# Kernel optimization log

Measured on AMD Instinct MI355X. Metric: run time of the kernel, lower is better.

The kernel has to match this reference:

```python
import jax, jax.numpy as jnp
import numpy as np

N_HEAD = 4

def setup_inputs() -> dict:
    key = jax.random.key(0)
    ks = jax.random.split(key, 5)
    B, T, C = 2, 4096, 64
    return {
        "x": jax.random.normal(ks[0], (B, T, C), dtype=jnp.float32),
        "w_attn": jax.random.normal(ks[1], (3 * C, C), dtype=jnp.float32) * 0.02,
        "b_attn": jax.random.normal(ks[2], (3 * C,), dtype=jnp.float32) * 0.02,
        "w_proj": jax.random.normal(ks[3], (C, C), dtype=jnp.float32) * 0.02,
        "b_proj": jax.random.normal(ks[4], (C,), dtype=jnp.float32) * 0.02,
    }

def reference(x, w_attn, b_attn, w_proj, b_proj):
    B, T, C = x.shape
    H = N_HEAD
    Dh = C // H
    # fused QKV projection (torch Linear: x @ W.T + b)
    qkv = x @ w_attn.T + b_attn                      # [B,T,3C]
    q, k, v = jnp.split(qkv, 3, axis=-1)             # each [B,T,C]
    q = q.reshape(B, T, H, Dh).transpose(0, 2, 1, 3)  # [B,H,T,Dh]
    k = k.reshape(B, T, H, Dh).transpose(0, 2, 1, 3)
    v = v.reshape(B, T, H, Dh).transpose(0, 2, 1, 3)
    scale = 1.0 / np.sqrt(Dh).astype(np.float32)
    scores = jnp.einsum("bhqd,bhkd->bhqk", q, k) * scale  # [B,H,T,T]
    attn = jax.nn.softmax(scores, axis=-1)
    y = jnp.einsum("bhqk,bhkd->bhqd", attn, v)       # [B,H,T,Dh]
    y = y.transpose(0, 2, 1, 3).reshape(B, T, C)     # [B,T,C]
    return y @ w_proj.T + b_proj
```

## Files before the change

### kernel.cpp

```cpp
#include <hip/hip_runtime.h>
#include <math.h>

#define BB 2
#define TT 4096
#define CC 64
#define HH 4
#define DH 16
#define NROW (BB*TT)
#define SCALE 0.36067376022224085f

typedef __fp16 h4 __attribute__((ext_vector_type(4)));
typedef __fp16 h2 __attribute__((ext_vector_type(2)));
typedef float  f4 __attribute__((ext_vector_type(4)));

__global__ __launch_bounds__(256) void qkv_kernel(const float* __restrict__ x,
        const float* __restrict__ w, const float* __restrict__ bias,
        __fp16* __restrict__ Q, __fp16* __restrict__ K, __fp16* __restrict__ VT) {
    __shared__ __fp16 smv[64][16];
    const int t = threadIdx.x;
    const int wave = t >> 6, lane = t & 63;
    const int lq = lane & 15, g = lane >> 4;
    const int r0 = blockIdx.x*16;
    const int b = r0 >> 12, tt0 = r0 & (TT-1);

    h4 xb[4];
    const float* xrow = x + (size_t)(r0 + lq)*CC;
    #pragma unroll
    for (int s = 0; s < 4; s++) {
        float4 xv = *(const float4*)(xrow + s*16 + g*4);
        h2 lo = __builtin_amdgcn_cvt_pkrtz(xv.x, xv.y);
        h2 hi = __builtin_amdgcn_cvt_pkrtz(xv.z, xv.w);
        xb[s] = (h4){lo.x, lo.y, hi.x, hi.y};
    }

    #pragma unroll
    for (int j = 0; j < 3; j++) {
        const int nt = wave*3 + j;
        const int o0 = nt*16;
        const float sc = (nt < 4) ? SCALE : 1.0f;
        float4 bv = *(const float4*)(bias + o0 + g*4);
        f4 acc = {bv.x*sc, bv.y*sc, bv.z*sc, bv.w*sc};
        #pragma unroll
        for (int s = 0; s < 4; s++) {
            float4 wv = *(const float4*)(w + (size_t)(o0 + lq)*CC + s*16 + g*4);
            h2 lo = __builtin_amdgcn_cvt_pkrtz(wv.x*sc, wv.y*sc);
            h2 hi = __builtin_amdgcn_cvt_pkrtz(wv.z*sc, wv.w*sc);
            h4 af = (h4){lo.x, lo.y, hi.x, hi.y};
            acc = __builtin_amdgcn_mfma_f32_16x16x16f16(af, xb[s], acc, 0, 0, 0);
        }
        h2 plo = __builtin_amdgcn_cvt_pkrtz(acc.x, acc.y);
        h2 phi = __builtin_amdgcn_cvt_pkrtz(acc.z, acc.w);
        h4 pk = (h4){plo.x, plo.y, phi.x, phi.y};
        if (nt < 8) {
            const int part = nt >> 2, h = nt & 3;
            __fp16* dst = (part == 0) ? Q : K;
            *(h4*)(dst + ((size_t)(b*HH + h)*TT + tt0 + lq)*DH + g*4) = pk;
        } else {
            const int h = nt - 8;
            smv[h*16 + g*4 + 0][lq] = pk.x;
            smv[h*16 + g*4 + 1][lq] = pk.y;
            smv[h*16 + g*4 + 2][lq] = pk.z;
            smv[h*16 + g*4 + 3][lq] = pk.w;
        }
    }
    __syncthreads();
    if (t < 64) {
        const int h = t >> 4, d = t & 15;
        uint4 v0 = *(const uint4*)&smv[t][0];
        uint4 v1 = *(const uint4*)&smv[t][8];
        __fp16* dst = VT + (size_t)(b*HH + h)*TT*DH
                        + (size_t)((tt0 >> 6)*16 + d)*64 + (tt0 & 63);
        *(uint4*)dst = v0;
        *(uint4*)(dst + 8) = v1;
    }
}

__global__ __launch_bounds__(256) void attn_kernel(const __fp16* __restrict__ Q,
        const __fp16* __restrict__ K, const __fp16* __restrict__ VT,
        __fp16* __restrict__ yh) {
    __shared__ f4    Osm[4][4][64];
    __shared__ float Lsm[4][4][64];
    const int t = threadIdx.x;
    const int wave = t >> 6, lane = t & 63;
    const int lq = lane & 15, g = lane >> 4;
    const int head = blockIdx.x >> 6;
    const int qt   = blockIdx.x & 63;
    const int q0 = qt*64;
    const __fp16* Qh = Q  + (size_t)head*TT*DH;
    const __fp16* Kh = K  + (size_t)head*TT*DH;
    const __fp16* Vh = VT + (size_t)head*TT*DH;

    h4 qf[4];
    #pragma unroll
    for (int h = 0; h < 4; h++)
        qf[h] = *(const h4*)(Qh + (size_t)(q0 + h*16 + lq)*DH + g*4);

    f4 O[4];
    float lp[4];
    #pragma unroll
    for (int h = 0; h < 4; h++) { O[h] = (f4){0.f,0.f,0.f,0.f}; lp[h] = 0.f; }

    const __fp16* kbase = Kh + (size_t)(wave*1024 + lq)*DH + g*4;
    const __fp16* vbase = Vh + (size_t)(wave*16)*1024 + lq*64 + g*4;

    const int start = (blockIdx.x*5 + wave*3) & 15;

    h4 ka[4], va[4], kb[4], vb[4];
    {
        const int c0 = start;
        #pragma unroll
        for (int s = 0; s < 4; s++) {
            ka[s] = *(const h4*)(kbase + (size_t)c0*64*DH + (size_t)s*16*DH);
            va[s] = *(const h4*)(vbase + (size_t)c0*1024 + s*16);
        }
    }

#define ATTN_CHUNK(KF, VF)                                                        \
    {                                                                             \
        const f4 z = {0.f, 0.f, 0.f, 0.f};                                        \
        _Pragma("unroll")                                                         \
        for (int h = 0; h < 4; h++) {                                             \
            f4 S0 = __builtin_amdgcn_mfma_f32_16x16x16f16(KF[0], qf[h], z, 0,0,0);\
            f4 S1 = __builtin_amdgcn_mfma_f32_16x16x16f16(KF[1], qf[h], z, 0,0,0);\
            f4 S2 = __builtin_amdgcn_mfma_f32_16x16x16f16(KF[2], qf[h], z, 0,0,0);\
            f4 S3 = __builtin_amdgcn_mfma_f32_16x16x16f16(KF[3], qf[h], z, 0,0,0);\
            float p0, p1, p2, p3; h2 lo, hi; h4 P; float lacc = 0.f;              \
            p0 = __builtin_amdgcn_exp2f(S0.x); p1 = __builtin_amdgcn_exp2f(S0.y); \
            p2 = __builtin_amdgcn_exp2f(S0.z); p3 = __builtin_amdgcn_exp2f(S0.w); \
            lacc += p0 + p1 + p2 + p3;                                            \
            lo = __builtin_amdgcn_cvt_pkrtz(p0, p1);                              \
            hi = __builtin_amdgcn_cvt_pkrtz(p2, p3);                              \
            P = (h4){lo.x, lo.y, hi.x, hi.y};                                     \
            O[h] = __builtin_amdgcn_mfma_f32_16x16x16f16(VF[0], P, O[h], 0,0,0);  \
            p0 = __builtin_amdgcn_exp2f(S1.x); p1 = __builtin_amdgcn_exp2f(S1.y); \
            p2 = __builtin_amdgcn_exp2f(S1.z); p3 = __builtin_amdgcn_exp2f(S1.w); \
            lacc += p0 + p1 + p2 + p3;                                            \
            lo = __builtin_amdgcn_cvt_pkrtz(p0, p1);                              \
            hi = __builtin_amdgcn_cvt_pkrtz(p2, p3);                              \
            P = (h4){lo.x, lo.y, hi.x, hi.y};                                     \
            O[h] = __builtin_amdgcn_mfma_f32_16x16x16f16(VF[1], P, O[h], 0,0,0);  \
            p0 = __builtin_amdgcn_exp2f(S2.x); p1 = __builtin_amdgcn_exp2f(S2.y); \
            p2 = __builtin_amdgcn_exp2f(S2.z); p3 = __builtin_amdgcn_exp2f(S2.w); \
            lacc += p0 + p1 + p2 + p3;                                            \
            lo = __builtin_amdgcn_cvt_pkrtz(p0, p1);                              \
            hi = __builtin_amdgcn_cvt_pkrtz(p2, p3);                              \
            P = (h4){lo.x, lo.y, hi.x, hi.y};                                     \
            O[h] = __builtin_amdgcn_mfma_f32_16x16x16f16(VF[2], P, O[h], 0,0,0);  \
            p0 = __builtin_amdgcn_exp2f(S3.x); p1 = __builtin_amdgcn_exp2f(S3.y); \
            p2 = __builtin_amdgcn_exp2f(S3.z); p3 = __builtin_amdgcn_exp2f(S3.w); \
            lacc += p0 + p1 + p2 + p3;                                            \
            lo = __builtin_amdgcn_cvt_pkrtz(p0, p1);                              \
            hi = __builtin_amdgcn_cvt_pkrtz(p2, p3);                              \
            P = (h4){lo.x, lo.y, hi.x, hi.y};                                     \
            O[h] = __builtin_amdgcn_mfma_f32_16x16x16f16(VF[3], P, O[h], 0,0,0);  \
            lp[h] += lacc;                                                        \
        }                                                                         \
    }

    for (int it = 0; it < 16; it += 2) {
        {
            const int c1 = (start + it + 1) & 15;
            #pragma unroll
            for (int s = 0; s < 4; s++) {
                kb[s] = *(const h4*)(kbase + (size_t)c1*64*DH + (size_t)s*16*DH);
                vb[s] = *(const h4*)(vbase + (size_t)c1*1024 + s*16);
            }
        }
        ATTN_CHUNK(ka, va)
        {
            const int c2 = (start + it + 2) & 15;
            #pragma unroll
            for (int s = 0; s < 4; s++) {
                ka[s] = *(const h4*)(kbase + (size_t)c2*64*DH + (size_t)s*16*DH);
                va[s] = *(const h4*)(vbase + (size_t)c2*1024 + s*16);
            }
        }
        ATTN_CHUNK(kb, vb)
    }
#undef ATTN_CHUNK

    #pragma unroll
    for (int h = 0; h < 4; h++) {
        Osm[wave][h][lane] = O[h];
        Lsm[wave][h][lane] = lp[h];
    }
    __syncthreads();

    f4 Os = Osm[0][wave][lane];
    Os += Osm[1][wave][lane];
    Os += Osm[2][wave][lane];
    Os += Osm[3][wave][lane];
    float L = 0.f;
    #pragma unroll
    for (int ks = 0; ks < 4; ks++)
        #pragma unroll
        for (int gg = 0; gg < 4; gg++)
            L += Lsm[ks][wave][gg*16 + lq];
    const float rinv = 1.f / L;
    h2 lo = __builtin_amdgcn_cvt_pkrtz(Os.x*rinv, Os.y*rinv);
    h2 hi = __builtin_amdgcn_cvt_pkrtz(Os.z*rinv, Os.w*rinv);
    h4 pk = (h4){lo.x, lo.y, hi.x, hi.y};
    const int b = head >> 2, hh = head & 3;
    *(h4*)(yh + ((size_t)b*TT + q0 + wave*16 + lq)*CC + hh*DH + g*4) = pk;
}

__global__ __launch_bounds__(256) void proj_kernel(const __fp16* __restrict__ yh,
        const float* __restrict__ w, const float* __restrict__ bias,
        float* __restrict__ out) {
    const int t = threadIdx.x;
    const int wave = t >> 6, lane = t & 63;
    const int lq = lane & 15, g = lane >> 4;
    const int r0 = blockIdx.x*16;
    const int o0 = wave*16;

    h4 yb[4];
    const __fp16* yrow = yh + (size_t)(r0 + lq)*CC;
    #pragma unroll
    for (int s = 0; s < 4; s++) yb[s] = *(const h4*)(yrow + s*16 + g*4);

    float4 bv = *(const float4*)(bias + o0 + g*4);
    f4 acc = {bv.x, bv.y, bv.z, bv.w};
    #pragma unroll
    for (int s = 0; s < 4; s++) {
        float4 wv = *(const float4*)(w + (size_t)(o0 + lq)*CC + s*16 + g*4);
        h2 lo = __builtin_amdgcn_cvt_pkrtz(wv.x, wv.y);
        h2 hi = __builtin_amdgcn_cvt_pkrtz(wv.z, wv.w);
        h4 af = (h4){lo.x, lo.y, hi.x, hi.y};
        acc = __builtin_amdgcn_mfma_f32_16x16x16f16(af, yb[s], acc, 0, 0, 0);
    }
    *(float4*)(out + (size_t)(r0 + lq)*CC + o0 + g*4) = (float4){acc.x, acc.y, acc.z, acc.w};
}

extern "C" void kernel_launch(void* const* d_in, const int* in_sizes, int n_in,
                              void* d_out, int out_size, void* d_ws, size_t ws_size,
                              hipStream_t stream) {
    const float* x      = (const float*)d_in[0];
    const float* w_attn = (const float*)d_in[1];
    const float* b_attn = (const float*)d_in[2];
    const float* w_proj = (const float*)d_in[3];
    const float* b_proj = (const float*)d_in[4];
    float* out = (float*)d_out;

    const size_t headsz = (size_t)BB*HH*TT*DH;
    __fp16* Q   = (__fp16*)d_ws;
    __fp16* K   = Q + headsz;
    __fp16* VT  = K + headsz;
    __fp16* yh  = VT + headsz;

    qkv_kernel<<<NROW/16, 256, 0, stream>>>(x, w_attn, b_attn, Q, K, VT);
    attn_kernel<<<BB*HH*(TT/64), 256, 0, stream>>>(Q, K, VT, yh);
    proj_kernel<<<NROW/16, 256, 0, stream>>>(yh, w_proj, b_proj, out);
}
```

Baseline: 95.16 us.

## Switch attention to 32x32x16 MFMA with ones-padded V for fused row sums

Rewrites the attention inner loop to use 32x32x16 f16 MFMA tiles instead of 16x16x16. S accumulators are rearranged into B-operand layout with v_permlane32_swap. The V^T buffer is padded to 32 rows per tile, with constant-one rows written in the qkv kernel, so the softmax denominator comes out of the PV MFMA instead of scalar adds. This aims to raise matrix throughput per instruction and drop the separate row-sum accumulation, at the cost of twice the V storage and bandwidth and wasted MFMA lanes on padding rows.

```diff
diff --git a/kernel.cpp b/kernel.cpp
--- a/kernel.cpp
+++ b/kernel.cpp
@@ -11,7 +11,12 @@
 
 typedef __fp16 h4 __attribute__((ext_vector_type(4)));
 typedef __fp16 h2 __attribute__((ext_vector_type(2)));
+typedef __fp16 h8 __attribute__((ext_vector_type(8)));
 typedef float  f4 __attribute__((ext_vector_type(4)));
+typedef float  f16v __attribute__((ext_vector_type(16)));
+
+union U4H8 { uint4 u; h8 h; };
+union UWH8 { unsigned u[4]; h8 h; };
 
 __global__ __launch_bounds__(256) void qkv_kernel(const float* __restrict__ x,
         const float* __restrict__ w, const float* __restrict__ bias,
@@ -68,140 +73,124 @@
         const int h = t >> 4, d = t & 15;
         uint4 v0 = *(const uint4*)&smv[t][0];
         uint4 v1 = *(const uint4*)&smv[t][8];
-        __fp16* dst = VT + (size_t)(b*HH + h)*TT*DH
-                        + (size_t)((tt0 >> 6)*16 + d)*64 + (tt0 & 63);
+        __fp16* dst = VT + (size_t)(b*HH + h)*TT*32
+                        + (size_t)(tt0 >> 6)*2048 + (size_t)d*64 + (tt0 & 63);
         *(uint4*)dst = v0;
         *(uint4*)(dst + 8) = v1;
+        const unsigned cb = (d == 0 || d == 4) ? 0x3C003C00u : 0u;
+        const uint4 cv = {cb, cb, cb, cb};
+        __fp16* dst2 = dst + 16*64;
+        *(uint4*)dst2 = cv;
+        *(uint4*)(dst2 + 8) = cv;
     }
 }
 
 __global__ __launch_bounds__(256) void attn_kernel(const __fp16* __restrict__ Q,
         const __fp16* __restrict__ K, const __fp16* __restrict__ VT,
         __fp16* __restrict__ yh) {
-    __shared__ f4    Osm[4][4][64];
-    __shared__ float Lsm[4][4][64];
+    __shared__ float Osm[4][2][64][9];
     const int t = threadIdx.x;
     const int wave = t >> 6, lane = t & 63;
-    const int lq = lane & 15, g = lane >> 4;
+    const int l31 = lane & 31, hi = lane >> 5;
     const int head = blockIdx.x >> 6;
     const int qt   = blockIdx.x & 63;
     const int q0 = qt*64;
     const __fp16* Qh = Q  + (size_t)head*TT*DH;
     const __fp16* Kh = K  + (size_t)head*TT*DH;
-    const __fp16* Vh = VT + (size_t)head*TT*DH;
-
-    h4 qf[4];
-    #pragma unroll
-    for (int h = 0; h < 4; h++)
-        qf[h] = *(const h4*)(Qh + (size_t)(q0 + h*16 + lq)*DH + g*4);
-
-    f4 O[4];
-    float lp[4];
-    #pragma unroll
-    for (int h = 0; h < 4; h++) { O[h] = (f4){0.f,0.f,0.f,0.f}; lp[h] = 0.f; }
-
-    const __fp16* kbase = Kh + (size_t)(wave*1024 + lq)*DH + g*4;
-    const __fp16* vbase = Vh + (size_t)(wave*16)*1024 + lq*64 + g*4;
+    const __fp16* Vh = VT + (size_t)head*TT*32;
+
+    U4H8 qf0, qf1;
+    qf0.u = *(const uint4*)(Qh + (size_t)(q0 + l31)*DH + hi*8);
+    qf1.u = *(const uint4*)(Qh + (size_t)(q0 + 32 + l31)*DH + hi*8);
+
+    const f16v Zf = {0.f,0.f,0.f,0.f,0.f,0.f,0.f,0.f,0.f,0.f,0.f,0.f,0.f,0.f,0.f,0.f};
+    f16v O0 = Zf, O1 = Zf;
+
+    const __fp16* kbase = Kh + (size_t)(wave*1024 + l31)*DH + hi*8;
+    const __fp16* vbase = Vh + (size_t)(wave*16)*2048 + l31*64 + hi*8;
 
     const int start = (blockIdx.x*5 + wave*3) & 15;
 
-    h4 ka[4], va[4], kb[4], vb[4];
-    {
-        const int c0 = start;
+    uint4 ka[2], va[4], kb[2], vb[4];
+
+#define LOADC(c, KF, VF)                                                   \
+    {  const size_t cc_ = (size_t)(c);                                     \
+       _Pragma("unroll") for (int kt_ = 0; kt_ < 2; kt_++)                 \
+           KF[kt_] = *(const uint4*)(kbase + cc_*1024 + kt_*512);          \
+       _Pragma("unroll") for (int s_ = 0; s_ < 4; s_++)                    \
+           VF[s_] = *(const uint4*)(vbase + cc_*2048 + s_*16);             \
+    }
+
+    LOADC(start, ka, va)
+
+#define PROC_TILE(S, O, VF)                                                        \
+    {   float p_[16]; unsigned W_[8];                                              \
+        _Pragma("unroll") for (int r_ = 0; r_ < 16; r_++)                          \
+            p_[r_] = __builtin_amdgcn_exp2f(S[r_]);                                \
+        _Pragma("unroll") for (int m_ = 0; m_ < 8; m_++)                           \
+            W_[m_] = __builtin_bit_cast(unsigned,                                  \
+                __builtin_amdgcn_cvt_pkrtz(p_[2*m_], p_[2*m_+1]));                 \
+        _Pragma("unroll") for (int s2 = 0; s2 < 2; s2++) {                         \
+            unsigned x0 = W_[4*s2+0], y0 = x0, x1 = W_[4*s2+1], y1 = x1;           \
+            unsigned x2 = W_[4*s2+2], y2 = x2, x3 = W_[4*s2+3], y3 = x3;           \
+            asm volatile("v_permlane32_swap_b32 %0, %1" : "+v"(x0), "+v"(y0));     \
+            asm volatile("v_permlane32_swap_b32 %0, %1" : "+v"(x1), "+v"(y1));     \
+            asm volatile("v_permlane32_swap_b32 %0, %1" : "+v"(x2), "+v"(y2));     \
+            asm volatile("v_permlane32_swap_b32 %0, %1" : "+v"(x3), "+v"(y3));     \
+            UWH8 bw_;                                                              \
+            bw_.u[0] = hi ? x2 : x0;  bw_.u[1] = hi ? x3 : x1;                     \
+            bw_.u[2] = hi ? y2 : y0;  bw_.u[3] = hi ? y3 : y1;                     \
+            U4H8 vv_; vv_.u = VF[kt*2+s2];                                         \
+            O = __builtin_amdgcn_mfma_f32_32x32x16_f16(vv_.h, bw_.h, O, 0,0,0);    \
+        }                                                                          \
+    }
+
+#define ATTN_CHUNK(KF, VF)                                                         \
+    _Pragma("unroll")                                                              \
+    for (int kt = 0; kt < 2; kt++) {                                               \
+        U4H8 ak_; ak_.u = KF[kt];                                                  \
+        f16v S0 = __builtin_amdgcn_mfma_f32_32x32x16_f16(ak_.h, qf0.h, Zf, 0,0,0); \
+        f16v S1 = __builtin_amdgcn_mfma_f32_32x32x16_f16(ak_.h, qf1.h, Zf, 0,0,0); \
+        PROC_TILE(S0, O0, VF)                                                      \
+        PROC_TILE(S1, O1, VF)                                                      \
+    }
+
+    for (int it = 0; it < 16; it += 2) {
+        LOADC((start + it + 1) & 15, kb, vb)
+        ATTN_CHUNK(ka, va)
+        LOADC((start + it + 2) & 15, ka, va)
+        ATTN_CHUNK(kb, vb)
+    }
+#undef ATTN_CHUNK
+#undef PROC_TILE
+#undef LOADC
+
+    #pragma unroll
+    for (int r = 0; r < 9; r++) {
+        Osm[wave][0][lane][r] = O0[r];
+        Osm[wave][1][lane][r] = O1[r];
+    }
+    __syncthreads();
+    if (wave < 2) {
+        const int qt2 = wave;
+        float a[9];
         #pragma unroll
-        for (int s = 0; s < 4; s++) {
-            ka[s] = *(const h4*)(kbase + (size_t)c0*64*DH + (size_t)s*16*DH);
-            va[s] = *(const h4*)(vbase + (size_t)c0*1024 + s*16);
-        }
-    }
-
-#define ATTN_CHUNK(KF, VF)                                                        \
-    {                                                                             \
-        const f4 z = {0.f, 0.f, 0.f, 0.f};                                        \
-        _Pragma("unroll")                                                         \
-        for (int h = 0; h < 4; h++) {                                             \
-            f4 S0 = __builtin_amdgcn_mfma_f32_16x16x16f16(KF[0], qf[h], z, 0,0,0);\
-            f4 S1 = __builtin_amdgcn_mfma_f32_16x16x16f16(KF[1], qf[h], z, 0,0,0);\
-            f4 S2 = __builtin_amdgcn_mfma_f32_16x16x16f16(KF[2], qf[h], z, 0,0,0);\
-            f4 S3 = __builtin_amdgcn_mfma_f32_16x16x16f16(KF[3], qf[h], z, 0,0,0);\
-            float p0, p1, p2, p3; h2 lo, hi; h4 P; float lacc = 0.f;              \
-            p0 = __builtin_amdgcn_exp2f(S0.x); p1 = __builtin_amdgcn_exp2f(S0.y); \
-            p2 = __builtin_amdgcn_exp2f(S0.z); p3 = __builtin_amdgcn_exp2f(S0.w); \
-            lacc += p0 + p1 + p2 + p3;                                            \
-            lo = __builtin_amdgcn_cvt_pkrtz(p0, p1);                              \
-            hi = __builtin_amdgcn_cvt_pkrtz(p2, p3);                              \
-            P = (h4){lo.x, lo.y, hi.x, hi.y};                                     \
-            O[h] = __builtin_amdgcn_mfma_f32_16x16x16f16(VF[0], P, O[h], 0,0,0);  \
-            p0 = __builtin_amdgcn_exp2f(S1.x); p1 = __builtin_amdgcn_exp2f(S1.y); \
-            p2 = __builtin_amdgcn_exp2f(S1.z); p3 = __builtin_amdgcn_exp2f(S1.w); \
-            lacc += p0 + p1 + p2 + p3;                                            \
-            lo = __builtin_amdgcn_cvt_pkrtz(p0, p1);                              \
-            hi = __builtin_amdgcn_cvt_pkrtz(p2, p3);                              \
-            P = (h4){lo.x, lo.y, hi.x, hi.y};                                     \
-            O[h] = __builtin_amdgcn_mfma_f32_16x16x16f16(VF[1], P, O[h], 0,0,0);  \
-            p0 = __builtin_amdgcn_exp2f(S2.x); p1 = __builtin_amdgcn_exp2f(S2.y); \
-            p2 = __builtin_amdgcn_exp2f(S2.z); p3 = __builtin_amdgcn_exp2f(S2.w); \
-            lacc += p0 + p1 + p2 + p3;                                            \
-            lo = __builtin_amdgcn_cvt_pkrtz(p0, p1);                              \
-            hi = __builtin_amdgcn_cvt_pkrtz(p2, p3);                              \
-            P = (h4){lo.x, lo.y, hi.x, hi.y};                                     \
-            O[h] = __builtin_amdgcn_mfma_f32_16x16x16f16(VF[2], P, O[h], 0,0,0);  \
-            p0 = __builtin_amdgcn_exp2f(S3.x); p1 = __builtin_amdgcn_exp2f(S3.y); \
-            p2 = __builtin_amdgcn_exp2f(S3.z); p3 = __builtin_amdgcn_exp2f(S3.w); \
-            lacc += p0 + p1 + p2 + p3;                                            \
-            lo = __builtin_amdgcn_cvt_pkrtz(p0, p1);                              \
-            hi = __builtin_amdgcn_cvt_pkrtz(p2, p3);                              \
-            P = (h4){lo.x, lo.y, hi.x, hi.y};                                     \
-            O[h] = __builtin_amdgcn_mfma_f32_16x16x16f16(VF[3], P, O[h], 0,0,0);  \
-            lp[h] += lacc;                                                        \
-        }                                                                         \
-    }
-
-    for (int it = 0; it < 16; it += 2) {
-        {
-            const int c1 = (start + it + 1) & 15;
-            #pragma unroll
-            for (int s = 0; s < 4; s++) {
-                kb[s] = *(const h4*)(kbase + (size_t)c1*64*DH + (size_t)s*16*DH);
-                vb[s] = *(const h4*)(vbase + (size_t)c1*1024 + s*16);
-            }
-        }
-        ATTN_CHUNK(ka, va)
-        {
-            const int c2 = (start + it + 2) & 15;
-            #pragma unroll
-            for (int s = 0; s < 4; s++) {
-                ka[s] = *(const h4*)(kbase + (size_t)c2*64*DH + (size_t)s*16*DH);
-                va[s] = *(const h4*)(vbase + (size_t)c2*1024 + s*16);
-            }
-        }
-        ATTN_CHUNK(kb, vb)
-    }
-#undef ATTN_CHUNK
-
-    #pragma unroll
-    for (int h = 0; h < 4; h++) {
-        Osm[wave][h][lane] = O[h];
-        Lsm[wave][h][lane] = lp[h];
-    }
-    __syncthreads();
-
-    f4 Os = Osm[0][wave][lane];
-    Os += Osm[1][wave][lane];
-    Os += Osm[2][wave][lane];
-    Os += Osm[3][wave][lane];
-    float L = 0.f;
-    #pragma unroll
-    for (int ks = 0; ks < 4; ks++)
-        #pragma unroll
-        for (int gg = 0; gg < 4; gg++)
-            L += Lsm[ks][wave][gg*16 + lq];
-    const float rinv = 1.f / L;
-    h2 lo = __builtin_amdgcn_cvt_pkrtz(Os.x*rinv, Os.y*rinv);
-    h2 hi = __builtin_amdgcn_cvt_pkrtz(Os.z*rinv, Os.w*rinv);
-    h4 pk = (h4){lo.x, lo.y, hi.x, hi.y};
-    const int b = head >> 2, hh = head & 3;
-    *(h4*)(yh + ((size_t)b*TT + q0 + wave*16 + lq)*CC + hh*DH + g*4) = pk;
+        for (int r = 0; r < 9; r++)
+            a[r] = Osm[0][qt2][lane][r] + Osm[1][qt2][lane][r]
+                 + Osm[2][qt2][lane][r] + Osm[3][qt2][lane][r];
+        const float rinv = 1.f / a[8];
+        h2 plo = __builtin_amdgcn_cvt_pkrtz(a[0]*rinv, a[1]*rinv);
+        h2 phi = __builtin_amdgcn_cvt_pkrtz(a[2]*rinv, a[3]*rinv);
+        h4 pk1 = (h4){plo.x, plo.y, phi.x, phi.y};
+        plo = __builtin_amdgcn_cvt_pkrtz(a[4]*rinv, a[5]*rinv);
+        phi = __builtin_amdgcn_cvt_pkrtz(a[6]*rinv, a[7]*rinv);
+        h4 pk2 = (h4){plo.x, plo.y, phi.x, phi.y};
+        const int b = head >> 2, hh = head & 3;
+        const size_t q = (size_t)q0 + qt2*32 + l31;
+        __fp16* dst = yh + ((size_t)b*TT + q)*CC + hh*DH + hi*4;
+        *(h4*)dst = pk1;
+        *(h4*)(dst + 8) = pk2;
+    }
 }
 
 __global__ __launch_bounds__(256) void proj_kernel(const __fp16* __restrict__ yh,
@@ -241,11 +230,12 @@
     const float* b_proj = (const float*)d_in[4];
     float* out = (float*)d_out;
 
-    const size_t headsz = (size_t)BB*HH*TT*DH;
+    const size_t headszQK = (size_t)BB*HH*TT*DH;
+    const size_t vtsz     = (size_t)BB*HH*TT*32;
     __fp16* Q   = (__fp16*)d_ws;
-    __fp16* K   = Q + headsz;
-    __fp16* VT  = K + headsz;
-    __fp16* yh  = VT + headsz;
+    __fp16* K   = Q + headszQK;
+    __fp16* VT  = K + headszQK;
+    __fp16* yh  = VT + vtsz;
 
     qkv_kernel<<<NROW/16, 256, 0, stream>>>(x, w_attn, b_attn, Q, K, VT);
     attn_kernel<<<BB*HH*(TT/64), 256, 0, stream>>>(Q, K, VT, yh);
```

After: 99.55 us. +4.6%, slower.
